# Kernel optimization log

Hardware: AMD Instinct MI355X
Metric: run time of the kernel (lower is better)

Reference implementation:

```python
import jax, jax.numpy as jnp
import numpy as np

B, T, C, H, D, S = 4096, 256, 64, 16, 16, 10


def setup_inputs() -> dict:
    key = jax.random.key(0)
    ks = jax.random.split(key, 8)
    return {
        'states_seq': jax.random.uniform(ks[0], (B, T, S), dtype=jnp.float32) + 0.5,
        'covariates_seq': jax.random.normal(ks[1], (B, T, C), dtype=jnp.float32),
        'ln_gamma': jnp.ones((C,), jnp.float32),
        'ln_beta': jnp.zeros((C,), jnp.float32),
        'rnn_wx': jax.random.normal(ks[2], (C, H), dtype=jnp.float32) * 0.1,
        'rnn_wh': jax.random.normal(ks[3], (H, H), dtype=jnp.float32) * 0.1,
        'rnn_b': jnp.zeros((H,), jnp.float32),
        'd1_w': jax.random.normal(ks[4], (H, H), dtype=jnp.float32) * 0.1,
        'd1_b': jnp.zeros((H,), jnp.float32),
        'd2_w': jax.random.normal(ks[5], (H, D), dtype=jnp.float32) * 0.1,
        'd2_b': jnp.zeros((D,), jnp.float32),
    }


def _cash_budget(s, d):
    # Deterministic cash-budget accounting update.
    # s: (B, 10) = [rev_prev, cash, AR, inventory, PPE, AP, debt, equity, retained, other]
    # d: (B, 16) drivers; first 10 used as ratios.
    sig = jax.nn.sigmoid
    g      = jnp.tanh(d[:, 0]) * 0.2      # sales growth
    cogs_m = sig(d[:, 1])                 # COGS margin
    opex_m = sig(d[:, 2]) * 0.5           # opex margin
    dep_r  = sig(d[:, 3]) * 0.1           # depreciation rate on PPE
    capex_r = sig(d[:, 4]) * 0.2          # capex as % of revenue
    dso = sig(d[:, 5])                    # AR ratio
    dio = sig(d[:, 6])                    # inventory ratio
    dpo = sig(d[:, 7])                    # AP ratio
    tax_r = sig(d[:, 8]) * 0.35           # tax rate
    int_r = sig(d[:, 9]) * 0.1            # interest rate on debt

    rev_prev, cash, ar, inv, ppe, ap, debt, equity, re, other = [s[:, i] for i in range(10)]
    rev = rev_prev * (1.0 + g)
    cogs = cogs_m * rev
    opex = opex_m * rev
    dep = dep_r * ppe
    interest = int_r * debt
    ebt = rev - cogs - opex - dep - interest
    tax = tax_r * jnp.maximum(ebt, 0.0)
    ni = ebt - tax
    ar_new = dso * rev
    inv_new = dio * cogs
    ap_new = dpo * cogs
    capex = capex_r * rev
    ppe_new = ppe + capex - dep
    cash_new = cash + ni + dep - capex - (ar_new - ar) - (inv_new - inv) + (ap_new - ap)
    re_new = re + ni
    s_next = jnp.stack([rev, cash_new, ar_new, inv_new, ppe_new, ap_new, debt, equity, re_new, other], axis=-1)
    is_out = jnp.stack([rev, cogs, opex, dep, interest, tax, ni], axis=-1)  # (B, 7)
    return s_next, is_out


def reference(states_seq, covariates_seq, ln_gamma, ln_beta, rnn_wx, rnn_wh, rnn_b, d1_w, d1_b, d2_w, d2_b):
    # LayerNormalization (keras default eps=1e-3, last axis)
    mu = covariates_seq.mean(-1, keepdims=True)
    var = covariates_seq.var(-1, keepdims=True)
    x = (covariates_seq - mu) * jax.lax.rsqrt(var + 1e-3) * ln_gamma + ln_beta

    # SimpleRNN: h_t = tanh(x_t Wx + h_{t-1} Wh + b), return_sequences
    xw = jnp.einsum('btc,ch->bth', x, rnn_wx) + rnn_b  # precompute input projection

    def rnn_step(h, xt):
        h = jnp.tanh(xt + h @ rnn_wh)
        return h, h

    h0 = jnp.zeros((x.shape[0], rnn_wh.shape[0]), x.dtype)
    _, hs = jax.lax.scan(rnn_step, h0, jnp.swapaxes(xw, 0, 1))  # (T, B, H)
    hs = jnp.swapaxes(hs, 0, 1)  # (B, T, H)

    drivers = jnp.tanh(hs @ d1_w + d1_b) @ d2_w + d2_b  # (B, T, D)

    # Cash-budget recurrence over t = 1 .. T-1
    def cb_step(s_prev, d_t):
        s_next, is_out = _cash_budget(s_prev, d_t)
        return s_next, (s_next, is_out)

    s0 = states_seq[:, 0, :]
    _, (states_tm, is_tm) = jax.lax.scan(cb_step, s0, jnp.swapaxes(drivers[:, 1:, :], 0, 1))
    states_pred = jnp.swapaxes(states_tm, 0, 1)  # (B, T-1, 10)
    is_pred = jnp.swapaxes(is_tm, 0, 1)          # (B, T-1, 7)
    return states_pred, is_pred
```

## Files before the change

kernel.cpp:

```cpp
#include <hip/hip_runtime.h>

#define NB 4096
#define NT 256
#define NC 64
#define NH 16
#define NS 10
#define NTO 255

__device__ __forceinline__ float fast_rcp(float x){
#if __has_builtin(__builtin_amdgcn_rcpf)
    return __builtin_amdgcn_rcpf(x);
#else
    return 1.0f/x;
#endif
}
__device__ __forceinline__ float fast_rsq(float x){
#if __has_builtin(__builtin_amdgcn_rsqf)
    return __builtin_amdgcn_rsqf(x);
#else
    return rsqrtf(x);
#endif
}
__device__ __forceinline__ float fsig(float x){
    return fast_rcp(1.0f + __expf(-x));
}
__device__ __forceinline__ float ftanh(float x){
    float e = __expf(2.0f*x);
    return fmaf(-2.0f, fast_rcp(e + 1.0f), 1.0f);
}

__global__ __launch_bounds__(64, 1) void vpf_kernel(
    const float* __restrict__ states, const float* __restrict__ cov,
    const float* __restrict__ lng,    const float* __restrict__ lnb,
    const float* __restrict__ wx,     const float* __restrict__ wh,
    const float* __restrict__ rnb,    const float* __restrict__ d1w,
    const float* __restrict__ d1b,    const float* __restrict__ d2w,
    const float* __restrict__ d2b,    float* __restrict__ out)
{
    const int lane = threadIdx.x;
    const int g = lane >> 4, l = lane & 15;
    const int b = (blockIdx.x << 2) + g;

    __shared__ __align__(16) float buf[2][4*NC];

    float gw[NC]; float Gs = 0.f, bacc = 0.f;
    #pragma unroll
    for (int c = 0; c < NC; ++c) {
        float w = wx[c*NH + l];
        float t = lng[c] * w;
        gw[c] = t; Gs += t;
        bacc = fmaf(lnb[c], w, bacc);
    }
    const float bwb = bacc + rnb[l];
    float whc[NH], d1c[NH], d2c[NH];
    #pragma unroll
    for (int k = 0; k < NH; ++k) {
        whc[k] = wh[k*NH + l];
        d1c[k] = d1w[k*NH + l];
        d2c[k] = d2w[k*NH + l];
    }
    const float d1bl = d1b[l], d2bl = d2b[l];

    float s0,s1,s2,s3,s4,s5,s6,s7,s8,s9;
    { const float* sp = states + (size_t)b*NT*NS;
      s0=sp[0];s1=sp[1];s2=sp[2];s3=sp[3];s4=sp[4];
      s5=sp[5];s6=sp[6];s7=sp[7];s8=sp[8];s9=sp[9]; }

    float* spo = out + (size_t)b*NTO*NS + l;
    float* ipo = out + (size_t)NB*NTO*NS + (size_t)b*NTO*7 + l;

    const float4* gp = (const float4*)(cov + (size_t)b*NT*NC) + l;
    float4 v0 = gp[0];
    float4 v1 = gp[16];
    float4 ra = gp[32];
    float4 rb = gp[48];
    ((float4*)buf[0])[lane] = v0;
    ((float4*)buf[1])[lane] = v1;
    __syncthreads();

    auto compute_xw = [&](const float* bp) -> float {
        const float4* row = (const float4*)(bp + g*NC);
        float4 ov = row[l];
        float ss = (ov.x+ov.y)+(ov.z+ov.w);
        float sq = fmaf(ov.x,ov.x, fmaf(ov.y,ov.y, fmaf(ov.z,ov.z, ov.w*ov.w)));
        #pragma unroll
        for (int m = 1; m < 16; m <<= 1) {
            ss += __shfl_xor(ss, m);
            sq += __shfl_xor(sq, m);
        }
        float mu  = ss * (1.0f/64.0f);
        float var = fmaf(-mu, mu, sq * (1.0f/64.0f));
        float rs  = fast_rsq(var + 0.001f);
        float a0=0.f, a1=0.f, a2=0.f, a3=0.f;
        #pragma unroll
        for (int c = 0; c < 16; ++c) {
            float4 v = row[c];
            a0 = fmaf(v.x, gw[4*c+0], a0);
            a1 = fmaf(v.y, gw[4*c+1], a1);
            a2 = fmaf(v.z, gw[4*c+2], a2);
            a3 = fmaf(v.w, gw[4*c+3], a3);
        }
        float dot = (a0+a1)+(a2+a3);
        return fmaf(rs, fmaf(-mu, Gs, dot), bwb);
    };

    float xw = compute_xw(buf[0]);
    float hrep[NH];
    #pragma unroll
    for (int j = 0; j < NH; ++j) hrep[j] = 0.f;
    const int base4 = (lane & 48) << 2;

    #pragma unroll 1
    for (int t = 0; t < NT; ++t) {
        if (t < NT-2) { ((float4*)buf[t&1])[lane] = ra; ra = rb; }
        if (t < NT-4) { rb = gp[(t+4)*16]; }
        float xwn = 0.f;
        if (t < NT-1) xwn = compute_xw(buf[(t+1)&1]);

        float a0 = xw, a1 = 0.f;
        #pragma unroll
        for (int k = 0; k < NH; k += 2) {
            a0 = fmaf(hrep[k],   whc[k],   a0);
            a1 = fmaf(hrep[k+1], whc[k+1], a1);
        }
        float hn = ftanh(a0 + a1);
        int hni = __float_as_int(hn);
        #pragma unroll
        for (int j = 0; j < NH; ++j)
            hrep[j] = __int_as_float(__builtin_amdgcn_ds_bpermute(base4 + 4*j, hni));

        if (t >= 1) {
            float b0 = d1bl, b1 = 0.f;
            #pragma unroll
            for (int k = 0; k < NH; k += 2) {
                b0 = fmaf(hrep[k],   d1c[k],   b0);
                b1 = fmaf(hrep[k+1], d1c[k+1], b1);
            }
            float t1 = ftanh(b0 + b1);
            int t1i = __float_as_int(t1);
            float t1rep[NH];
            #pragma unroll
            for (int j = 0; j < NH; ++j)
                t1rep[j] = __int_as_float(__builtin_amdgcn_ds_bpermute(base4 + 4*j, t1i));
            float c0 = d2bl, c1 = 0.f;
            #pragma unroll
            for (int k = 0; k < NH; k += 2) {
                c0 = fmaf(t1rep[k],   d2c[k],   c0);
                c1 = fmaf(t1rep[k+1], d2c[k+1], c1);
            }
            float dv = c0 + c1;
            int dvi = __float_as_int(dv);
            float dd[10];
            #pragma unroll
            for (int j = 0; j < 10; ++j)
                dd[j] = __int_as_float(__builtin_amdgcn_ds_bpermute(base4 + 4*j, dvi));

            float gg    = 0.2f  * ftanh(dd[0]);
            float cogsm = fsig(dd[1]);
            float opexm = 0.5f  * fsig(dd[2]);
            float depr  = 0.1f  * fsig(dd[3]);
            float capr  = 0.2f  * fsig(dd[4]);
            float dso   = fsig(dd[5]);
            float dio   = fsig(dd[6]);
            float dpo   = fsig(dd[7]);
            float taxr  = 0.35f * fsig(dd[8]);
            float intr  = 0.1f  * fsig(dd[9]);

            float rev   = fmaf(s0, gg, s0);
            float cogs  = cogsm * rev;
            float opex  = opexm * rev;
            float dep   = depr * s4;
            float inte  = intr * s6;
            float ebt   = (((rev - cogs) - opex) - dep) - inte;
            float tax   = taxr * fmaxf(ebt, 0.0f);
            float ni    = ebt - tax;
            float arn   = dso * rev;
            float invn  = dio * cogs;
            float apn   = dpo * cogs;
            float capex = capr * rev;
            float ppen  = (s4 + capex) - dep;
            float cashn = (((((s1 + ni) + dep) - capex) - (arn - s2)) - (invn - s3)) + (apn - s5);
            float ren   = s8 + ni;

            s0=rev; s1=cashn; s2=arn; s3=invn; s4=ppen; s5=apn; s8=ren;

            float sv = (l==0)?rev:(l==1)?cashn:(l==2)?arn:(l==3)?invn:(l==4)?ppen:
                       (l==5)?apn:(l==6)?s6:(l==7)?s7:(l==8)?ren:s9;
            float iv = (l==0)?rev:(l==1)?cogs:(l==2)?opex:(l==3)?dep:(l==4)?inte:(l==5)?tax:ni;
            if (l < NS) *spo = sv;
            if (l < 7)  *ipo = iv;
            spo += NS; ipo += 7;
        }
        xw = xwn;
        __syncthreads();
    }
}

extern "C" void kernel_launch(void* const* d_in, const int* in_sizes, int n_in,
                              void* d_out, int out_size, void* d_ws, size_t ws_size,
                              hipStream_t stream) {
    (void)in_sizes; (void)n_in; (void)d_ws; (void)ws_size; (void)out_size;
    vpf_kernel<<<NB/4, 64, 0, stream>>>(
        (const float*)d_in[0],
        (const float*)d_in[1],
        (const float*)d_in[2],
        (const float*)d_in[3],
        (const float*)d_in[4],
        (const float*)d_in[5],
        (const float*)d_in[6],
        (const float*)d_in[7],
        (const float*)d_in[8],
        (const float*)d_in[9],
        (const float*)d_in[10],
        (float*)d_out);
}
```

Measured before the change: 685.7 us.

## Split input projection into separate fp16 kernel and use DPP rotations in scan

The layernorm plus input projection moves into its own highly parallel kernel that writes xw to workspace in half precision. The recurrent scan kernel then only reads these precomputed values. The 16-wide matvecs now use DPP row rotations with pre-rotated weights instead of ds_bpermute broadcasts. The driver activations are also computed per lane with a unified sigmoid form and shared through LDS. In exchange, the fp16 storage of xw reduces precision, and an extra launch plus a workspace round trip are added.

New measurement: 598.6 us. 1.15x faster.

```diff
diff --git a/kernel.cpp b/kernel.cpp
--- a/kernel.cpp
+++ b/kernel.cpp
@@ -1,4 +1,5 @@
 #include <hip/hip_runtime.h>
+#include <hip/hip_fp16.h>
 
 #define NB 4096
 #define NT 256
@@ -7,33 +8,107 @@
 #define NS 10
 #define NTO 255
 
-__device__ __forceinline__ float fast_rcp(float x){
-#if __has_builtin(__builtin_amdgcn_rcpf)
-    return __builtin_amdgcn_rcpf(x);
-#else
-    return 1.0f/x;
-#endif
-}
-__device__ __forceinline__ float fast_rsq(float x){
-#if __has_builtin(__builtin_amdgcn_rsqf)
-    return __builtin_amdgcn_rsqf(x);
-#else
-    return rsqrtf(x);
-#endif
-}
-__device__ __forceinline__ float fsig(float x){
-    return fast_rcp(1.0f + __expf(-x));
-}
+__device__ __forceinline__ float fast_rcp(float x){ return __builtin_amdgcn_rcpf(x); }
+__device__ __forceinline__ float fast_rsq(float x){ return __builtin_amdgcn_rsqf(x); }
+__device__ __forceinline__ float fsig(float x){ return fast_rcp(1.0f + __expf(-x)); }
 __device__ __forceinline__ float ftanh(float x){
     float e = __expf(2.0f*x);
     return fmaf(-2.0f, fast_rcp(e + 1.0f), 1.0f);
 }
 
-__global__ __launch_bounds__(64, 1) void vpf_kernel(
-    const float* __restrict__ states, const float* __restrict__ cov,
-    const float* __restrict__ lng,    const float* __restrict__ lnb,
-    const float* __restrict__ wx,     const float* __restrict__ wh,
-    const float* __restrict__ rnb,    const float* __restrict__ d1w,
+template<int R>
+__device__ __forceinline__ float rotf(float x){
+    return __int_as_float(__builtin_amdgcn_update_dpp(
+        0, __float_as_int(x), 0x120 + R, 0xF, 0xF, true));
+}
+__device__ __forceinline__ float row_bcast_sum(float x){
+    x += rotf<8>(x);
+    x += rotf<4>(x);
+    x += rotf<2>(x);
+    x += rotf<1>(x);
+    return x;
+}
+__device__ __forceinline__ float rotdot16(float v, const float* w, float acc){
+    float a1 = 0.f;
+    acc = fmaf(v,          w[0],  acc);
+    a1  = fmaf(rotf<1>(v), w[1],  a1);
+    acc = fmaf(rotf<2>(v), w[2],  acc);
+    a1  = fmaf(rotf<3>(v), w[3],  a1);
+    acc = fmaf(rotf<4>(v), w[4],  acc);
+    a1  = fmaf(rotf<5>(v), w[5],  a1);
+    acc = fmaf(rotf<6>(v), w[6],  acc);
+    a1  = fmaf(rotf<7>(v), w[7],  a1);
+    acc = fmaf(rotf<8>(v), w[8],  acc);
+    a1  = fmaf(rotf<9>(v), w[9],  a1);
+    acc = fmaf(rotf<10>(v),w[10], acc);
+    a1  = fmaf(rotf<11>(v),w[11], a1);
+    acc = fmaf(rotf<12>(v),w[12], acc);
+    a1  = fmaf(rotf<13>(v),w[13], a1);
+    acc = fmaf(rotf<14>(v),w[14], acc);
+    a1  = fmaf(rotf<15>(v),w[15], a1);
+    return acc + a1;
+}
+
+__global__ __launch_bounds__(256, 4) void xw_kernel(
+    const float* __restrict__ cov, const float* __restrict__ lng,
+    const float* __restrict__ lnb, const float* __restrict__ wx,
+    const float* __restrict__ rnb, __half* __restrict__ xws)
+{
+    const int wid  = threadIdx.x >> 6;
+    const int lane = threadIdx.x & 63;
+    const int g = lane >> 4, l = lane & 15;
+    const int b = (blockIdx.x << 2) + wid;
+
+    float gwr[64];
+    #pragma unroll
+    for (int r = 0; r < 16; ++r) {
+        int c0 = 4 * ((l - r) & 15);
+        #pragma unroll
+        for (int j = 0; j < 4; ++j)
+            gwr[4*r+j] = lng[c0+j] * wx[(c0+j)*NH + l];
+    }
+    float bwb = rnb[l];
+    #pragma unroll
+    for (int c = 0; c < NC; ++c) bwb = fmaf(lnb[c], wx[c*NH + l], bwb);
+
+    const float4* gp = (const float4*)cov + (size_t)b*NT*16 + g*16 + l;
+    __half* op = xws + ((size_t)b*16 + l)*NT + g;
+
+    float4 cur = gp[0];
+    float4 nxt = gp[64];
+    #pragma unroll 2
+    for (int it = 0; it < 64; ++it) {
+        float4 x = cur;
+        cur = nxt;
+        if (it < 62) nxt = gp[(size_t)(it+2)*64];
+        float ss = (x.x + x.y) + (x.z + x.w);
+        float sq = fmaf(x.x,x.x, fmaf(x.y,x.y, fmaf(x.z,x.z, x.w*x.w)));
+        ss = row_bcast_sum(ss);
+        sq = row_bcast_sum(sq);
+        float mu  = ss * (1.0f/64.0f);
+        float var = fmaf(-mu, mu, sq * (1.0f/64.0f));
+        float rs  = fast_rsq(var + 0.001f);
+        float nmu = -mu * rs;
+        float x0 = fmaf(x.x, rs, nmu), x1 = fmaf(x.y, rs, nmu);
+        float x2 = fmaf(x.z, rs, nmu), x3 = fmaf(x.w, rs, nmu);
+        float a0 = bwb, a1 = 0.f, a2 = 0.f, a3 = 0.f;
+        a0 = fmaf(x0, gwr[0], a0); a1 = fmaf(x1, gwr[1], a1);
+        a2 = fmaf(x2, gwr[2], a2); a3 = fmaf(x3, gwr[3], a3);
+#define ROTSTEP(R) { float r0=rotf<R>(x0), r1=rotf<R>(x1), r2=rotf<R>(x2), r3=rotf<R>(x3); \
+        a0=fmaf(r0,gwr[4*R+0],a0); a1=fmaf(r1,gwr[4*R+1],a1); \
+        a2=fmaf(r2,gwr[4*R+2],a2); a3=fmaf(r3,gwr[4*R+3],a3); }
+        ROTSTEP(1)  ROTSTEP(2)  ROTSTEP(3)  ROTSTEP(4)  ROTSTEP(5)
+        ROTSTEP(6)  ROTSTEP(7)  ROTSTEP(8)  ROTSTEP(9)  ROTSTEP(10)
+        ROTSTEP(11) ROTSTEP(12) ROTSTEP(13) ROTSTEP(14) ROTSTEP(15)
+#undef ROTSTEP
+        float xw = (a0+a1)+(a2+a3);
+        op[it*4] = __float2half(xw);
+    }
+}
+
+__global__ __launch_bounds__(64, 1) void scan_kernel(
+    const float* __restrict__ states, const __half* __restrict__ xws,
+    const float* __restrict__ wh,     const float* __restrict__ d1w,
     const float* __restrict__ d1b,    const float* __restrict__ d2w,
     const float* __restrict__ d2b,    float* __restrict__ out)
 {
@@ -41,25 +116,20 @@
     const int g = lane >> 4, l = lane & 15;
     const int b = (blockIdx.x << 2) + g;
 
-    __shared__ __align__(16) float buf[2][4*NC];
-
-    float gw[NC]; float Gs = 0.f, bacc = 0.f;
+    __shared__ __align__(16) float db[64];
+
+    float whr[NH], d1r[NH], d2r[NH];
     #pragma unroll
-    for (int c = 0; c < NC; ++c) {
-        float w = wx[c*NH + l];
-        float t = lng[c] * w;
-        gw[c] = t; Gs += t;
-        bacc = fmaf(lnb[c], w, bacc);
-    }
-    const float bwb = bacc + rnb[l];
-    float whc[NH], d1c[NH], d2c[NH];
-    #pragma unroll
-    for (int k = 0; k < NH; ++k) {
-        whc[k] = wh[k*NH + l];
-        d1c[k] = d1w[k*NH + l];
-        d2c[k] = d2w[k*NH + l];
+    for (int r = 0; r < NH; ++r) {
+        int src = (l - r) & 15;
+        whr[r] = wh[src*NH + l];
+        d1r[r] = d1w[src*NH + l];
+        d2r[r] = d2w[src*NH + l];
     }
     const float d1bl = d1b[l], d2bl = d2b[l];
+    const float Aa = (l==0)?0.4f:(l==2)?0.5f:(l==3)?0.1f:(l==4)?0.2f:(l==8)?0.35f:(l==9)?0.1f:1.0f;
+    const float Ba = (l==0)?2.0f:1.0f;
+    const float Ca = (l==0)?-0.2f:0.0f;
 
     float s0,s1,s2,s3,s4,s5,s6,s7,s8,s9;
     { const float* sp = states + (size_t)b*NT*NS;
@@ -69,145 +139,73 @@
     float* spo = out + (size_t)b*NTO*NS + l;
     float* ipo = out + (size_t)NB*NTO*NS + (size_t)b*NTO*7 + l;
 
-    const float4* gp = (const float4*)(cov + (size_t)b*NT*NC) + l;
-    float4 v0 = gp[0];
-    float4 v1 = gp[16];
-    float4 ra = gp[32];
-    float4 rb = gp[48];
-    ((float4*)buf[0])[lane] = v0;
-    ((float4*)buf[1])[lane] = v1;
-    __syncthreads();
-
-    auto compute_xw = [&](const float* bp) -> float {
-        const float4* row = (const float4*)(bp + g*NC);
-        float4 ov = row[l];
-        float ss = (ov.x+ov.y)+(ov.z+ov.w);
-        float sq = fmaf(ov.x,ov.x, fmaf(ov.y,ov.y, fmaf(ov.z,ov.z, ov.w*ov.w)));
+    const ushort4* xp = (const ushort4*)(xws + ((size_t)b*16 + l)*NT);
+    ushort4 xa = xp[0], xb = xp[1];
+
+    float h = 0.f;
+    #pragma unroll 1
+    for (int tt = 0; tt < 64; ++tt) {
+        ushort4 xc = xa; xa = xb;
+        if (tt < 62) xb = xp[tt+2];
         #pragma unroll
-        for (int m = 1; m < 16; m <<= 1) {
-            ss += __shfl_xor(ss, m);
-            sq += __shfl_xor(sq, m);
+        for (int u = 0; u < 4; ++u) {
+            const int t = tt*4 + u;
+            float xwv = __half2float(__ushort_as_half(u==0?xc.x:u==1?xc.y:u==2?xc.z:xc.w));
+            h = ftanh(rotdot16(h, whr, xwv));
+            if (t > 0) {
+                float t1  = ftanh(rotdot16(h, d1r, d1bl));
+                float dv  = rotdot16(t1, d2r, d2bl);
+                float act = fmaf(Aa, fsig(Ba * dv), Ca);
+                db[lane] = act;
+                float4 w0 = *((const float4*)db + g*4);
+                float4 w1 = *((const float4*)db + g*4 + 1);
+                float2 w2 = *((const float2*)(db + g*16 + 8));
+
+                float rev   = fmaf(s0, w0.x, s0);
+                float cogs  = w0.y * rev;
+                float opex  = w0.z * rev;
+                float dep   = w0.w * s4;
+                float inte  = w2.y * s6;
+                float ebt   = (((rev - cogs) - opex) - dep) - inte;
+                float tax   = w2.x * fmaxf(ebt, 0.0f);
+                float ni    = ebt - tax;
+                float arn   = w1.y * rev;
+                float invn  = w1.z * cogs;
+                float apn   = w1.w * cogs;
+                float capex = w1.x * rev;
+                float ppen  = (s4 + capex) - dep;
+                float cashn = (((((s1 + ni) + dep) - capex) - (arn - s2)) - (invn - s3)) + (apn - s5);
+                float ren   = s8 + ni;
+
+                s0=rev; s1=cashn; s2=arn; s3=invn; s4=ppen; s5=apn; s8=ren;
+
+                float sv = (l==0)?rev:(l==1)?cashn:(l==2)?arn:(l==3)?invn:(l==4)?ppen:
+                           (l==5)?apn:(l==6)?s6:(l==7)?s7:(l==8)?ren:s9;
+                float iv = (l==0)?rev:(l==1)?cogs:(l==2)?opex:(l==3)?dep:(l==4)?inte:(l==5)?tax:ni;
+                if (l < NS) *spo = sv;
+                if (l < 7)  *ipo = iv;
+                spo += NS; ipo += 7;
+            }
         }
-        float mu  = ss * (1.0f/64.0f);
-        float var = fmaf(-mu, mu, sq * (1.0f/64.0f));
-        float rs  = fast_rsq(var + 0.001f);
-        float a0=0.f, a1=0.f, a2=0.f, a3=0.f;
-        #pragma unroll
-        for (int c = 0; c < 16; ++c) {
-            float4 v = row[c];
-            a0 = fmaf(v.x, gw[4*c+0], a0);
-            a1 = fmaf(v.y, gw[4*c+1], a1);
-            a2 = fmaf(v.z, gw[4*c+2], a2);
-            a3 = fmaf(v.w, gw[4*c+3], a3);
-        }
-        float dot = (a0+a1)+(a2+a3);
-        return fmaf(rs, fmaf(-mu, Gs, dot), bwb);
-    };
-
-    float xw = compute_xw(buf[0]);
-    float hrep[NH];
-    #pragma unroll
-    for (int j = 0; j < NH; ++j) hrep[j] = 0.f;
-    const int base4 = (lane & 48) << 2;
-
-    #pragma unroll 1
-    for (int t = 0; t < NT; ++t) {
-        if (t < NT-2) { ((float4*)buf[t&1])[lane] = ra; ra = rb; }
-        if (t < NT-4) { rb = gp[(t+4)*16]; }
-        float xwn = 0.f;
-        if (t < NT-1) xwn = compute_xw(buf[(t+1)&1]);
-
-        float a0 = xw, a1 = 0.f;
-        #pragma unroll
-        for (int k = 0; k < NH; k += 2) {
-            a0 = fmaf(hrep[k],   whc[k],   a0);
-            a1 = fmaf(hrep[k+1], whc[k+1], a1);
-        }
-        float hn = ftanh(a0 + a1);
-        int hni = __float_as_int(hn);
-        #pragma unroll
-        for (int j = 0; j < NH; ++j)
-            hrep[j] = __int_as_float(__builtin_amdgcn_ds_bpermute(base4 + 4*j, hni));
-
-        if (t >= 1) {
-            float b0 = d1bl, b1 = 0.f;
-            #pragma unroll
-            for (int k = 0; k < NH; k += 2) {
-                b0 = fmaf(hrep[k],   d1c[k],   b0);
-                b1 = fmaf(hrep[k+1], d1c[k+1], b1);
-            }
-            float t1 = ftanh(b0 + b1);
-            int t1i = __float_as_int(t1);
-            float t1rep[NH];
-            #pragma unroll
-            for (int j = 0; j < NH; ++j)
-                t1rep[j] = __int_as_float(__builtin_amdgcn_ds_bpermute(base4 + 4*j, t1i));
-            float c0 = d2bl, c1 = 0.f;
-            #pragma unroll
-            for (int k = 0; k < NH; k += 2) {
-                c0 = fmaf(t1rep[k],   d2c[k],   c0);
-                c1 = fmaf(t1rep[k+1], d2c[k+1], c1);
-            }
-            float dv = c0 + c1;
-            int dvi = __float_as_int(dv);
-            float dd[10];
-            #pragma unroll
-            for (int j = 0; j < 10; ++j)
-                dd[j] = __int_as_float(__builtin_amdgcn_ds_bpermute(base4 + 4*j, dvi));
-
-            float gg    = 0.2f  * ftanh(dd[0]);
-            float cogsm = fsig(dd[1]);
-            float opexm = 0.5f  * fsig(dd[2]);
-            float depr  = 0.1f  * fsig(dd[3]);
-            float capr  = 0.2f  * fsig(dd[4]);
-            float dso   = fsig(dd[5]);
-            float dio   = fsig(dd[6]);
-            float dpo   = fsig(dd[7]);
-            float taxr  = 0.35f * fsig(dd[8]);
-            float intr  = 0.1f  * fsig(dd[9]);
-
-            float rev   = fmaf(s0, gg, s0);
-            float cogs  = cogsm * rev;
-            float opex  = opexm * rev;
-            float dep   = depr * s4;
-            float inte  = intr * s6;
-            float ebt   = (((rev - cogs) - opex) - dep) - inte;
-            float tax   = taxr * fmaxf(ebt, 0.0f);
-            float ni    = ebt - tax;
-            float arn   = dso * rev;
-            float invn  = dio * cogs;
-            float apn   = dpo * cogs;
-            float capex = capr * rev;
-            float ppen  = (s4 + capex) - dep;
-            float cashn = (((((s1 + ni) + dep) - capex) - (arn - s2)) - (invn - s3)) + (apn - s5);
-            float ren   = s8 + ni;
-
-            s0=rev; s1=cashn; s2=arn; s3=invn; s4=ppen; s5=apn; s8=ren;
-
-            float sv = (l==0)?rev:(l==1)?cashn:(l==2)?arn:(l==3)?invn:(l==4)?ppen:
-                       (l==5)?apn:(l==6)?s6:(l==7)?s7:(l==8)?ren:s9;
-            float iv = (l==0)?rev:(l==1)?cogs:(l==2)?opex:(l==3)?dep:(l==4)?inte:(l==5)?tax:ni;
-            if (l < NS) *spo = sv;
-            if (l < 7)  *ipo = iv;
-            spo += NS; ipo += 7;
-        }
-        xw = xwn;
-        __syncthreads();
     }
 }
 
 extern "C" void kernel_launch(void* const* d_in, const int* in_sizes, int n_in,
                               void* d_out, int out_size, void* d_ws, size_t ws_size,
                               hipStream_t stream) {
-    (void)in_sizes; (void)n_in; (void)d_ws; (void)ws_size; (void)out_size;
-    vpf_kernel<<<NB/4, 64, 0, stream>>>(
-        (const float*)d_in[0],
+    (void)in_sizes; (void)n_in; (void)ws_size; (void)out_size;
+    __half* xws = (__half*)d_ws;
+    xw_kernel<<<NB/4, 256, 0, stream>>>(
         (const float*)d_in[1],
         (const float*)d_in[2],
         (const float*)d_in[3],
         (const float*)d_in[4],
+        (const float*)d_in[6],
+        xws);
+    scan_kernel<<<NB/4, 64, 0, stream>>>(
+        (const float*)d_in[0],
+        xws,
         (const float*)d_in[5],
-        (const float*)d_in[6],
         (const float*)d_in[7],
         (const float*)d_in[8],
         (const float*)d_in[9],
```
